# Performance work log

Hardware: AMD Instinct MI355X
Metric: run time of the kernel (lower is better)

## Reference

```python
import jax, jax.numpy as jnp
import numpy as np

EMBED_DIM = 256
NUM_HEADS = 8
HEAD_DIM = EMBED_DIM // NUM_HEADS
SCALING = HEAD_DIM ** -0.5
SEQ = 1024
BSZ = 4


def setup_inputs() -> dict:
    rng = jax.random.key(0)
    ks = jax.random.split(rng, 5)
    E = EMBED_DIM
    q = jax.random.normal(ks[0], (SEQ, BSZ, E), jnp.float32)
    k = jax.random.normal(ks[1], (SEQ, BSZ, E), jnp.float32)
    v = jax.random.normal(ks[2], (SEQ, BSZ, E), jnp.float32)
    # xavier-uniform-like scale for the packed 9E x E projection
    lim_in = np.sqrt(6.0 / (9 * E + E)).astype(np.float32)
    in_proj_w = jax.random.uniform(ks[3], (9 * E, E), jnp.float32, -lim_in, lim_in)
    in_proj_b = jnp.zeros((9 * E,), jnp.float32)
    lim_out = np.sqrt(6.0 / (E + E)).astype(np.float32)
    out_w = jax.random.uniform(ks[4], (E, E), jnp.float32, -lim_out, lim_out)
    out_b = jnp.zeros((E,), jnp.float32)
    return {"query": q, "key": k, "value": v,
            "in_proj_w": in_proj_w, "in_proj_b": in_proj_b,
            "out_w": out_w, "out_b": out_b,
            "shape0": 32, "shape1": 32}


def reference(query, key, value, in_proj_w, in_proj_b, out_w, out_b, shape0, shape1):
    S, B, E = query.shape
    H, hd = NUM_HEADS, HEAD_DIM

    def proj(x, i):  # slice i of the packed in-projection
        return x @ in_proj_w[i * E:(i + 1) * E].T + in_proj_b[i * E:(i + 1) * E]

    def heads(x):  # [S,B,E] -> [B*H, S, hd]
        return x.reshape(S, B * H, hd).transpose(1, 0, 2)

    q      = heads(proj(query, 0) * SCALING)
    k      = heads(proj(key, 1))
    v      = heads(proj(value, 2))
    q_left = heads(proj(query, 3))
    k_left = heads(proj(key, 4))
    q_right = heads(proj(query, 5))
    k_right = heads(proj(key, 6))
    q_loc  = heads(proj(query, 7) * SCALING)
    k_loc  = heads(proj(key, 8))

    global_w = q @ k.transpose(0, 2, 1)        # [BH,S,S]
    local_w  = q_loc @ k_loc.transpose(0, 2, 1)

    left_sm  = jax.nn.softmax(q_left @ k_left.transpose(0, 2, 1), axis=-1)
    right_sm = jax.nn.softmax(q_right @ k_right.transpose(0, 2, 1), axis=-1)

    triu = jnp.triu(jnp.ones((S, S), query.dtype))
    mini = jnp.tile(jnp.triu(jnp.ones((shape1, shape1), query.dtype)), (shape0, shape0))
    triu = (triu * mini)[None]                 # [1,S,S]
    triu_t = triu.transpose(0, 2, 1)

    fw_mask = (left_sm @ triu) * (right_sm @ triu_t)
    bw_mask = (left_sm @ triu_t) * (right_sm @ triu)
    local_mask = fw_mask + bw_mask             # [BH,S,S]

    attn_w = jax.nn.softmax(0.1 * global_w + local_w * local_mask, axis=-1)
    attn = (attn_w @ v).transpose(1, 0, 2).reshape(S, B, E)
    attn = attn @ out_w.T + out_b
    consistent_mask = local_mask.sum(axis=0)   # [S,S]
    return attn, consistent_mask
```

## Files before the change

### kernel.cpp

```cpp
#include <hip/hip_runtime.h>


typedef _Float16 v8h __attribute__((ext_vector_type(8)));
typedef _Float16 v4h __attribute__((ext_vector_type(4)));
typedef _Float16 v2h __attribute__((ext_vector_type(2)));
typedef float    v4f __attribute__((ext_vector_type(4)));

#define SL 1048576
#define RS 1032

static constexpr float SCALE = 0.17677669529663687f;


__global__ __launch_bounds__(256)
void cvt_kernel(const float* __restrict__ q, const float* __restrict__ k,
                const float* __restrict__ v, const float* __restrict__ W,
                _Float16* __restrict__ X16, _Float16* __restrict__ W16)
{
    const int b = blockIdx.x;
    const int t = threadIdx.x;
    const float* src; _Float16* dst; int off;
    if (b < 512)       { src = q; dst = X16;             off = b; }
    else if (b < 1024) { src = k; dst = X16 + (1 << 20); off = b - 512; }
    else if (b < 1536) { src = v; dst = X16 + (2 << 20); off = b - 1024; }
    else               { src = W; dst = W16;             off = b - 1536; }
    const int i = off * 2048 + t * 8;
    const float4 a = *(const float4*)(src + i);
    const float4 c = *(const float4*)(src + i + 4);
    v8h h;
    h[0] = (_Float16)a.x; h[1] = (_Float16)a.y; h[2] = (_Float16)a.z; h[3] = (_Float16)a.w;
    h[4] = (_Float16)c.x; h[5] = (_Float16)c.y; h[6] = (_Float16)c.z; h[7] = (_Float16)c.w;
    *(v8h*)(dst + i) = h;
}

__global__ __launch_bounds__(256)
void proj_kernel(const _Float16* __restrict__ X16, const _Float16* __restrict__ W16,
                 const float* __restrict__ bias, _Float16* __restrict__ P)
{
    __shared__ __align__(16) _Float16 stage[4096];
    const int t  = threadIdx.x;
    const int n0 = blockIdx.x * 64;
    const int m0 = blockIdx.y * 64;
    const int slice = n0 >> 8;
    const int q2 = (n0 >> 6) & 3;
    const bool kslice = (slice == 1) || (slice == 4) || (slice == 6) || (slice == 8);
    const _Float16* X = X16 + (slice == 2 ? (2 << 20) : (kslice ? (1 << 20) : 0));
    const int w = t >> 6, lane = t & 63, m16 = lane & 15, kg = lane >> 4;
    const v4f zero = {0.f, 0.f, 0.f, 0.f};
    v4f acc[4] = {zero, zero, zero, zero};
    const _Float16* Arow = X + (size_t)(m0 + w * 16 + m16) * 256 + kg * 8;
    const _Float16* B0   = W16 + (size_t)(n0 + m16) * 256 + kg * 8;
#pragma unroll
    for (int kk = 0; kk < 8; ++kk) {
        const v8h a = *(const v8h*)(Arow + kk * 32);
#pragma unroll
        for (int nf = 0; nf < 4; ++nf) {
            const v8h bb = *(const v8h*)(B0 + nf * 4096 + kk * 32);
            acc[nf] = __builtin_amdgcn_mfma_f32_16x16x32_f16(a, bb, acc[nf], 0, 0, 0);
        }
    }
    const float scale = (slice == 0 || slice == 7) ? SCALE : 1.0f;
#pragma unroll
    for (int nf = 0; nf < 4; ++nf) {
        const int c = n0 + nf * 16 + m16;
        const float bv = bias[c];
#pragma unroll
        for (int i = 0; i < 4; ++i) {
            const _Float16 val = (_Float16)((acc[nf][i] + bv) * scale);
            const int lb = i * 2 + (nf >> 1);
            int inner;
            if (slice == 2) {
                const int ls = w * 4 + kg;
                inner = ((nf & 1) << 8) + ((ls >> 3) << 7) + m16 * 8 + (ls & 7);
            } else {
                inner = ((w * 4 + kg) + (((nf & 1) * 2 + (m16 >> 3)) << 4)) * 8 + (m16 & 7);
            }
            stage[lb * 512 + inner] = val;
        }
    }
    __syncthreads();
    {
        const int o  = t * 16;
        const int lb = o >> 9;
        const int inner = o & 511;
        const int bs = lb >> 1, hh = lb & 1;
        const int bh = bs * 8 + 2 * q2 + hh;
        size_t dst;
        if (slice == 2) {
            const int kc = m0 >> 7;
            const int g0 = (m0 >> 5) & 3;
            const int nt = inner >> 8, a = (inner >> 7) & 1, r = inner & 127;
            dst = (size_t)2 * SL + (size_t)bh * 32768
                + (size_t)(kc * 1024 + nt * 512 + (g0 + a) * 128 + r);
        } else {
            const int tile = m0 >> 6;
            dst = (size_t)slice * SL + (size_t)bh * 32768 + (size_t)(tile * 512 + inner);
        }
        *(v8h*)(P + dst)     = *(const v8h*)(stage + o);
        *(v8h*)(P + dst + 8) = *(const v8h*)(stage + o + 8);
    }
}

__global__ __launch_bounds__(512, 4)
void attn_kernel(const _Float16* __restrict__ P, float* __restrict__ attn_pre,
                 _Float16* __restrict__ pmask)
{
    __shared__ __align__(16) _Float16 Lh[16 * RS];
    __shared__ __align__(16) _Float16 Rh[16 * RS];
    __shared__ __align__(16) _Float16 Ledge[16][36];
    __shared__ __align__(16) _Float16 Redge[16][36];

    const int t    = threadIdx.x;
    const int bid  = blockIdx.x;
    const int q    = bid >> 3;
    const int bh   = ((bid & 7) << 2) + (q & 3);
    const int rt   = q >> 2;
    const int w    = __builtin_amdgcn_readfirstlane(t >> 6);
    const int lane = t & 63;
    const int m16  = lane & 15;
    const int kg   = lane >> 4;

    const _Float16* Pb = P + (size_t)bh * 32768;
    const v4f zero = {0.f, 0.f, 0.f, 0.f};

    {
        const v8h a_l = *(const v8h*)(Pb + 3 * SL + rt * 512 + lane * 8);
        const v8h a_r = *(const v8h*)(Pb + 5 * SL + rt * 512 + lane * 8);
        const _Float16* Bl = Pb + 4 * SL;
        const _Float16* Br = Pb + 6 * SL;
#pragma unroll 4
        for (int jt2 = 0; jt2 < 8; ++jt2) {
            const int jt = (w << 3) + jt2;
            const v8h bL = *(const v8h*)(Bl + jt * 512 + lane * 8);
            const v8h bR = *(const v8h*)(Br + jt * 512 + lane * 8);
            v4f cL = __builtin_amdgcn_mfma_f32_16x16x32_f16(bL, a_l, zero, 0, 0, 0);
            v4f cR = __builtin_amdgcn_mfma_f32_16x16x32_f16(bR, a_r, zero, 0, 0, 0);
            v4h hL, hR;
#pragma unroll
            for (int i = 0; i < 4; ++i) { hL[i] = (_Float16)cL[i]; hR[i] = (_Float16)cR[i]; }
            const int base = m16 * RS + (jt << 4) + (kg << 2);
            *(v4h*)&Lh[base] = hL;
            *(v4h*)&Rh[base] = hR;
        }
    }
    __syncthreads();

    {
        const int kr = lane & 31;
        for (int r = 0; r < 2; ++r) {
            const int row = (w << 1) + r;
            _Float16* ROW = (lane >= 32) ? &Rh[row * RS] : &Lh[row * RS];
            float x[32];
#pragma unroll
            for (int kb = 0; kb < 32; ++kb)
                x[kb] = __expf((float)ROW[(kb << 5) + kr]);
#pragma unroll
            for (int kb = 0; kb < 32; ++kb) {
#pragma unroll
                for (int off = 1; off < 32; off <<= 1) {
                    const float y = __shfl_up(x[kb], off, 32);
                    if (kr >= off) x[kb] += y;
                }
            }
#pragma unroll
            for (int kb = 1; kb < 32; ++kb) x[kb] += x[kb - 1];
            const float inv = 1.f / __shfl(x[31], 31, 32);
            _Float16* EG = (lane >= 32) ? &Redge[row][0] : &Ledge[row][0];
            EG[kr + 1] = (_Float16)(x[31] * inv);
            if (kr == 0) EG[0] = (_Float16)0.f;
#pragma unroll
            for (int kb = 0; kb < 32; ++kb)
                ROW[(kb << 5) + kr] = (_Float16)(x[kb] * inv);
        }
    }
    __syncthreads();

    v4h sc4[8];
    {
        _Float16* pm = pmask + (size_t)bh * 1048576 + (size_t)rt * 16384;
        const v8h a_g = *(const v8h*)(Pb + 0 * SL + rt * 512 + lane * 8);
        const v8h a_c = *(const v8h*)(Pb + 7 * SL + rt * 512 + lane * 8);
        const _Float16* Bg = Pb + 1 * SL;
        const _Float16* Bc = Pb + 8 * SL;
        const int rr = m16 * RS;
#pragma unroll
        for (int jt2 = 0; jt2 < 8; ++jt2) {
            const int jt   = (w << 3) + jt2;
            const int jb   = jt >> 1;
            const int jr0  = ((jt & 1) << 4) + (kg << 2);
            const int colb = (jt << 4) + (kg << 2);
            const v8h bG = *(const v8h*)(Bg + jt * 512 + lane * 8);
            const v8h bC = *(const v8h*)(Bc + jt * 512 + lane * 8);
            const v4f g4 = __builtin_amdgcn_mfma_f32_16x16x32_f16(bG, a_g, zero, 0, 0, 0);
            const v4f l4 = __builtin_amdgcn_mfma_f32_16x16x32_f16(bC, a_c, zero, 0, 0, 0);
            const v4h PLv  = *(const v4h*)&Lh[rr + colb];
            const v4h PRv  = *(const v4h*)&Rh[rr + colb];
            const v4h eLcv = *(const v4h*)&Ledge[m16][jr0];
            const v4h eRcv = *(const v4h*)&Redge[m16][jr0];
            float eLb = 0.f, eRb = 0.f;
            if (jb) {
                eLb = (float)Lh[rr + (jb << 5) - 1];
                eRb = (float)Rh[rr + (jb << 5) - 1];
            }
            v4h s4, m4;
#pragma unroll
            for (int i = 0; i < 4; ++i) {
                const int jrv = jr0 + i;
                const float PL  = (float)PLv[i];
                const float PR  = (float)PRv[i];
                const float eLc = (float)eLcv[i];
                const float eRc = (float)eRcv[i];
                float eLbc = 0.f, eRbc = 0.f;
                if (jb && jrv) {
                    const int o = rr + ((jb - 1) << 5) + jrv - 1;
                    eLbc = (float)Lh[o];
                    eRbc = (float)Rh[o];
                }
                const float SLv = 1.0f - eLb - eLc + eLbc;
                const float SRv = 1.0f - eRb - eRc + eRbc;
                const float mkv = PL * SRv + SLv * PR;
                s4[i] = (_Float16)(0.1f * g4[i] + l4[i] * mkv);
                m4[i] = (_Float16)mkv;
            }
            sc4[jt2] = s4;
            *(v4h*)(pm + ((size_t)jt << 8) + (m16 << 4) + (kg << 2)) = m4;
        }
    }
    __syncthreads();

    {
#pragma unroll
        for (int jt2 = 0; jt2 < 8; ++jt2)
            *(v4h*)&Lh[m16 * RS + (((w << 3) + jt2) << 4) + (kg << 2)] = sc4[jt2];
    }
    __syncthreads();

    auto softmax_pairs = [&](_Float16* ROW) {
        float v0[8], v1[8];
        float ss = 0.f;
#pragma unroll
        for (int kq = 0; kq < 8; ++kq) {
            const v2h pr = *(const v2h*)&ROW[(lane + (kq << 6)) << 1];
            v0[kq] = __expf((float)pr[0]);
            v1[kq] = __expf((float)pr[1]);
            ss += v0[kq] + v1[kq];
        }
#pragma unroll
        for (int off = 32; off; off >>= 1) ss += __shfl_xor(ss, off);
        const float inv = 1.f / ss;
#pragma unroll
        for (int kq = 0; kq < 8; ++kq) {
            v2h pr; pr[0] = (_Float16)(v0[kq] * inv); pr[1] = (_Float16)(v1[kq] * inv);
            *(v2h*)&ROW[(lane + (kq << 6)) << 1] = pr;
        }
    };
#pragma unroll
    for (int r = 0; r < 2; ++r) softmax_pairs(&Lh[((w << 1) + r) * RS]);
    __syncthreads();

    {
        const int nt = w & 1, hf = w >> 1;
        v4f c = zero;
        const _Float16* Vb = Pb + 2 * SL + nt * 512 + lane * 8;
        const int kc0 = hf << 3;
#pragma unroll 4
        for (int kc2 = 0; kc2 < 8; ++kc2) {
            const int kc = kc0 + kc2;
            const v8h a = *(const v8h*)&Lh[m16 * RS + (kc << 5) + (kg << 3)];
            const v8h b = *(const v8h*)(Vb + (size_t)kc * 1024);
            c = __builtin_amdgcn_mfma_f32_16x16x32_f16(a, b, c, 0, 0, 0);
        }
        float* Pbuf = (float*)&Rh[0];
#pragma unroll
        for (int i = 0; i < 4; ++i) Pbuf[(w << 8) + (lane << 2) + i] = c[i];
    }
    __syncthreads();

    {
        const float* Pbuf = (const float*)&Rh[0];
        const int r   = t >> 5;
        const int d   = t & 31;
        const int nt2 = d >> 4, n = d & 15;
        const int kg2 = r >> 2, i2 = r & 3;
        const int off = (kg2 << 6) + (n << 2) + i2;
        float v = 0.f;
#pragma unroll
        for (int hf = 0; hf < 4; ++hf)
            v += Pbuf[(((hf << 1) + nt2) << 8) + off];
        const int srow = (rt << 4) + r;
        attn_pre[((size_t)(srow * 4 + (bh >> 3))) * 256 + (bh & 7) * 32 + d] = v;
    }
}

__global__ __launch_bounds__(256)
void tail_kernel(const _Float16* __restrict__ pmask, float* __restrict__ cmask,
                 const float* __restrict__ A, const float* __restrict__ W,
                 const float* __restrict__ bias, float* __restrict__ C)
{
    __shared__ __align__(16) float SMEM[4 * 16 * 136];
    const int bid = blockIdx.x;
    const int t = threadIdx.x;

    if (bid >= 256) {
        const int b2 = bid - 256;
        const int rt = b2 >> 3, wh = b2 & 7;
        float (*T4)[16][136] = (float(*)[16][136])SMEM;
        const int wv = t >> 6;
        const int lane = t & 63;
        float acc[8][4] = {};
        const _Float16* base = pmask + (size_t)rt * 16384 + ((size_t)wh << 11) + (lane << 2)
                             + ((size_t)wv << 3) * 1048576;
        for (int bh = 0; bh < 8; ++bh) {
            const _Float16* p = base + (size_t)bh * 1048576;
#pragma unroll
            for (int jt2 = 0; jt2 < 8; ++jt2) {
                const v4h h4 = *(const v4h*)(p + (jt2 << 8));
#pragma unroll
                for (int i = 0; i < 4; ++i) acc[jt2][i] += (float)h4[i];
            }
        }
#pragma unroll
        for (int jt2 = 0; jt2 < 8; ++jt2)
#pragma unroll
            for (int i = 0; i < 4; ++i)
                T4[wv][lane >> 2][(jt2 << 4) + ((lane & 3) << 2) + i] = acc[jt2][i];
        __syncthreads();
        const int row = t >> 4;
        const int c0  = (t & 15) << 3;
#pragma unroll
        for (int h = 0; h < 2; ++h) {
            const int c = c0 + (h << 2);
            const float4 s0 = *(const float4*)&T4[0][row][c];
            const float4 s1 = *(const float4*)&T4[1][row][c];
            const float4 s2 = *(const float4*)&T4[2][row][c];
            const float4 s3 = *(const float4*)&T4[3][row][c];
            const float4 o = make_float4(s0.x + s1.x + s2.x + s3.x,
                                         s0.y + s1.y + s2.y + s3.y,
                                         s0.z + s1.z + s2.z + s3.z,
                                         s0.w + s1.w + s2.w + s3.w);
            *(float4*)&cmask[((size_t)((rt << 4) + row) << 10) + (wh << 7) + c] = o;
        }
    } else {
        const int n0 = (bid & 3) * 64;
        const int m0 = (bid >> 2) * 64;
        float (*As)[68] = (float(*)[68])SMEM;
        float (*Bs)[68] = (float(*)[68])(SMEM + 16 * 68);
        const int tx = t & 15, ty = t >> 4;
        const int lm = t >> 2, lk = (t & 3) << 2;
        float acc[4][4] = {};
        for (int k0 = 0; k0 < 256; k0 += 16) {
            float4 av = *(const float4*)(A + (size_t)(m0 + lm) * 256 + k0 + lk);
            float4 bv = *(const float4*)(W + (size_t)(n0 + lm) * 256 + k0 + lk);
            As[lk + 0][lm] = av.x; As[lk + 1][lm] = av.y; As[lk + 2][lm] = av.z; As[lk + 3][lm] = av.w;
            Bs[lk + 0][lm] = bv.x; Bs[lk + 1][lm] = bv.y; Bs[lk + 2][lm] = bv.z; Bs[lk + 3][lm] = bv.w;
            __syncthreads();
#pragma unroll
            for (int kk = 0; kk < 16; ++kk) {
                float4 a4 = *(const float4*)&As[kk][ty << 2];
                float4 b4 = *(const float4*)&Bs[kk][tx << 2];
                float aa[4] = {a4.x, a4.y, a4.z, a4.w};
                float bb[4] = {b4.x, b4.y, b4.z, b4.w};
#pragma unroll
                for (int i = 0; i < 4; ++i)
#pragma unroll
                    for (int j = 0; j < 4; ++j)
                        acc[i][j] = fmaf(aa[i], bb[j], acc[i][j]);
            }
            __syncthreads();
        }
#pragma unroll
        for (int i = 0; i < 4; ++i) {
            const int m  = m0 + (ty << 2) + i;
            const int c0 = n0 + (tx << 2);
            float4 o = make_float4(acc[i][0] + bias[c0 + 0], acc[i][1] + bias[c0 + 1],
                                   acc[i][2] + bias[c0 + 2], acc[i][3] + bias[c0 + 3]);
            *(float4*)&C[(size_t)m * 256 + c0] = o;
        }
    }
}

extern "C" void kernel_launch(void* const* d_in, const int* in_sizes, int n_in,
                              void* d_out, int out_size, void* d_ws, size_t ws_size,
                              hipStream_t stream)
{
    const float* q  = (const float*)d_in[0];
    const float* k  = (const float*)d_in[1];
    const float* v  = (const float*)d_in[2];
    const float* Wi = (const float*)d_in[3];
    const float* bi = (const float*)d_in[4];
    const float* Wo = (const float*)d_in[5];
    const float* bo = (const float*)d_in[6];

    float* out      = (float*)d_out;
    float* attn_out = out;
    float* cmask    = out + 1048576;

    _Float16* Ppack    = (_Float16*)d_ws;
    float*    attn_pre = (float*)((char*)d_ws + 18874368);
    _Float16* pmask    = (_Float16*)((char*)d_ws + 23068672);
    _Float16* X16      = (_Float16*)((char*)d_ws + 90177536);
    _Float16* W16      = (_Float16*)((char*)d_ws + 96468992);

    cvt_kernel<<<1824, 256, 0, stream>>>(q, k, v, Wi, X16, W16);
    proj_kernel<<<dim3(36, 64), 256, 0, stream>>>(X16, W16, bi, Ppack);
    attn_kernel<<<2048, 512, 0, stream>>>(Ppack, attn_pre, pmask);
    tail_kernel<<<768, 256, 0, stream>>>(pmask, cmask, attn_pre, Wo, bo, attn_out);
}
```

Measured before the change: 260.7 us.

## Fuse softmax exp into score computation and widen projection tiles to 128 columns

The attention kernel now exponentiates scores while computing them, accumulates per-row partial sums across lanes and waves through a small shared buffer, and writes normalized probabilities once. This removes a shared-memory round trip, one barrier, and the separate softmax pass. It drops the max-subtraction, so large logits could overflow in fp16. Separately, the projection kernel computes 128 output columns per block instead of 64, halving the grid and reusing each A fragment across twice as many MFMAs.

```diff
diff --git a/kernel.cpp b/kernel.cpp
--- a/kernel.cpp
+++ b/kernel.cpp
@@ -37,37 +37,37 @@
 void proj_kernel(const _Float16* __restrict__ X16, const _Float16* __restrict__ W16,
                  const float* __restrict__ bias, _Float16* __restrict__ P)
 {
-    __shared__ __align__(16) _Float16 stage[4096];
+    __shared__ __align__(16) _Float16 stage[8192];
     const int t  = threadIdx.x;
-    const int n0 = blockIdx.x * 64;
+    const int n0 = blockIdx.x * 128;
     const int m0 = blockIdx.y * 64;
     const int slice = n0 >> 8;
-    const int q2 = (n0 >> 6) & 3;
+    const int q4 = (n0 >> 7) & 1;
     const bool kslice = (slice == 1) || (slice == 4) || (slice == 6) || (slice == 8);
     const _Float16* X = X16 + (slice == 2 ? (2 << 20) : (kslice ? (1 << 20) : 0));
     const int w = t >> 6, lane = t & 63, m16 = lane & 15, kg = lane >> 4;
     const v4f zero = {0.f, 0.f, 0.f, 0.f};
-    v4f acc[4] = {zero, zero, zero, zero};
+    v4f acc[8] = {zero, zero, zero, zero, zero, zero, zero, zero};
     const _Float16* Arow = X + (size_t)(m0 + w * 16 + m16) * 256 + kg * 8;
     const _Float16* B0   = W16 + (size_t)(n0 + m16) * 256 + kg * 8;
 #pragma unroll
     for (int kk = 0; kk < 8; ++kk) {
         const v8h a = *(const v8h*)(Arow + kk * 32);
 #pragma unroll
-        for (int nf = 0; nf < 4; ++nf) {
+        for (int nf = 0; nf < 8; ++nf) {
             const v8h bb = *(const v8h*)(B0 + nf * 4096 + kk * 32);
             acc[nf] = __builtin_amdgcn_mfma_f32_16x16x32_f16(a, bb, acc[nf], 0, 0, 0);
         }
     }
     const float scale = (slice == 0 || slice == 7) ? SCALE : 1.0f;
 #pragma unroll
-    for (int nf = 0; nf < 4; ++nf) {
+    for (int nf = 0; nf < 8; ++nf) {
         const int c = n0 + nf * 16 + m16;
         const float bv = bias[c];
 #pragma unroll
         for (int i = 0; i < 4; ++i) {
             const _Float16 val = (_Float16)((acc[nf][i] + bv) * scale);
-            const int lb = i * 2 + (nf >> 1);
+            const int lb = i * 4 + (nf >> 1);
             int inner;
             if (slice == 2) {
                 const int ls = w * 4 + kg;
@@ -80,24 +80,25 @@
     }
     __syncthreads();
     {
-        const int o  = t * 16;
+        const int o  = t * 32;
         const int lb = o >> 9;
         const int inner = o & 511;
-        const int bs = lb >> 1, hh = lb & 1;
-        const int bh = bs * 8 + 2 * q2 + hh;
+        const int bs = lb >> 2, hh = lb & 3;
+        const int bh = bs * 8 + q4 * 4 + hh;
         size_t dst;
         if (slice == 2) {
             const int kc = m0 >> 7;
             const int g0 = (m0 >> 5) & 3;
-            const int nt = inner >> 8, a = (inner >> 7) & 1, r = inner & 127;
+            const int nt = inner >> 8, a2 = (inner >> 7) & 1, r = inner & 127;
             dst = (size_t)2 * SL + (size_t)bh * 32768
-                + (size_t)(kc * 1024 + nt * 512 + (g0 + a) * 128 + r);
+                + (size_t)(kc * 1024 + nt * 512 + (g0 + a2) * 128 + r);
         } else {
             const int tile = m0 >> 6;
             dst = (size_t)slice * SL + (size_t)bh * 32768 + (size_t)(tile * 512 + inner);
         }
-        *(v8h*)(P + dst)     = *(const v8h*)(stage + o);
-        *(v8h*)(P + dst + 8) = *(const v8h*)(stage + o + 8);
+#pragma unroll
+        for (int h8 = 0; h8 < 4; ++h8)
+            *(v8h*)(P + dst + h8 * 8) = *(const v8h*)(stage + o + h8 * 8);
     }
 }
 
@@ -109,6 +110,7 @@
     __shared__ __align__(16) _Float16 Rh[16 * RS];
     __shared__ __align__(16) _Float16 Ledge[16][36];
     __shared__ __align__(16) _Float16 Redge[16][36];
+    __shared__ float Zp[8][16];
 
     const int t    = threadIdx.x;
     const int bid  = blockIdx.x;
@@ -175,7 +177,8 @@
     }
     __syncthreads();
 
-    v4h sc4[8];
+    v4h p4[8];
+    float psum = 0.f;
     {
         _Float16* pm = pmask + (size_t)bh * 1048576 + (size_t)rt * 16384;
         const v8h a_g = *(const v8h*)(Pb + 0 * SL + rt * 512 + lane * 8);
@@ -202,7 +205,7 @@
                 eLb = (float)Lh[rr + (jb << 5) - 1];
                 eRb = (float)Rh[rr + (jb << 5) - 1];
             }
-            v4h s4, m4;
+            v4h m4;
 #pragma unroll
             for (int i = 0; i < 4; ++i) {
                 const int jrv = jr0 + i;
@@ -219,43 +222,32 @@
                 const float SLv = 1.0f - eLb - eLc + eLbc;
                 const float SRv = 1.0f - eRb - eRc + eRbc;
                 const float mkv = PL * SRv + SLv * PR;
-                s4[i] = (_Float16)(0.1f * g4[i] + l4[i] * mkv);
+                const float pv  = __expf(0.1f * g4[i] + l4[i] * mkv);
+                p4[jt2][i] = (_Float16)pv;
+                psum += pv;
                 m4[i] = (_Float16)mkv;
             }
-            sc4[jt2] = s4;
             *(v4h*)(pm + ((size_t)jt << 8) + (m16 << 4) + (kg << 2)) = m4;
         }
-    }
-    __syncthreads();
-
-    {
-#pragma unroll
-        for (int jt2 = 0; jt2 < 8; ++jt2)
-            *(v4h*)&Lh[m16 * RS + (((w << 3) + jt2) << 4) + (kg << 2)] = sc4[jt2];
-    }
-    __syncthreads();
-
-    auto softmax_pairs = [&](_Float16* ROW) {
-        float v0[8], v1[8];
-        float ss = 0.f;
-#pragma unroll
-        for (int kq = 0; kq < 8; ++kq) {
-            const v2h pr = *(const v2h*)&ROW[(lane + (kq << 6)) << 1];
-            v0[kq] = __expf((float)pr[0]);
-            v1[kq] = __expf((float)pr[1]);
-            ss += v0[kq] + v1[kq];
-        }
-#pragma unroll
-        for (int off = 32; off; off >>= 1) ss += __shfl_xor(ss, off);
-        const float inv = 1.f / ss;
-#pragma unroll
-        for (int kq = 0; kq < 8; ++kq) {
-            v2h pr; pr[0] = (_Float16)(v0[kq] * inv); pr[1] = (_Float16)(v1[kq] * inv);
-            *(v2h*)&ROW[(lane + (kq << 6)) << 1] = pr;
-        }
-    };
-#pragma unroll
-    for (int r = 0; r < 2; ++r) softmax_pairs(&Lh[((w << 1) + r) * RS]);
+        psum += __shfl_xor(psum, 16);
+        psum += __shfl_xor(psum, 32);
+        if (lane < 16) Zp[w][m16] = psum;
+    }
+    __syncthreads();
+
+    {
+        float Z = 0.f;
+#pragma unroll
+        for (int w8 = 0; w8 < 8; ++w8) Z += Zp[w8][m16];
+        const float inv = 1.f / Z;
+#pragma unroll
+        for (int jt2 = 0; jt2 < 8; ++jt2) {
+            v4h o;
+#pragma unroll
+            for (int i = 0; i < 4; ++i) o[i] = (_Float16)((float)p4[jt2][i] * inv);
+            *(v4h*)&Lh[m16 * RS + (((w << 3) + jt2) << 4) + (kg << 2)] = o;
+        }
+    }
     __syncthreads();
 
     {
@@ -402,7 +394,7 @@
     _Float16* W16      = (_Float16*)((char*)d_ws + 96468992);
 
     cvt_kernel<<<1824, 256, 0, stream>>>(q, k, v, Wi, X16, W16);
-    proj_kernel<<<dim3(36, 64), 256, 0, stream>>>(X16, W16, bi, Ppack);
+    proj_kernel<<<dim3(18, 64), 256, 0, stream>>>(X16, W16, bi, Ppack);
     attn_kernel<<<2048, 512, 0, stream>>>(Ppack, attn_pre, pmask);
     tail_kernel<<<768, 256, 0, stream>>>(pmask, cmask, attn_pre, Wo, bo, attn_out);
 }
```

Result: no change. 257.0 us (-1.4%).
